# Kernel tuning notes

Measured on AMD Instinct MI355X. Metric: run time of the kernel, lower is better.

Reference implementation:

```python
import jax, jax.numpy as jnp
import numpy as np

D2 = 200  # 2*100 hardcoded in BiAttentionLayer.__init__
NEG = -10000000.0


def masked_softmax(v, m):
    # Faithful to the torch masked_softmax: softmax(v * m), re-mask, renormalize.
    r = jax.nn.softmax(v * m, axis=-1)
    r = r * m
    return r / (jnp.sum(r, axis=-1, keepdims=True) + 1e-13)


def setup_inputs() -> dict:
    key = jax.random.key(0)
    k0, k1, k2, k3, k4, k5 = jax.random.split(key, 6)
    N, T, J = 64, 1024, 64
    H = jax.random.normal(k0, (N, T, D2), jnp.float32)
    U = jax.random.normal(k1, (N, J, D2), jnp.float32)
    c_mask = jax.random.randint(k2, (N, T), 0, 2).astype(jnp.float32)
    q_mask = jax.random.randint(k3, (N, J), 0, 2).astype(jnp.float32)
    w = jax.random.normal(k4, (3 * D2,), jnp.float32) * 0.05  # Linear(3*d2, 1) weight
    b = jax.random.normal(k5, (), jnp.float32) * 0.05          # Linear bias
    return {"H": H, "U": U, "c_mask": c_mask, "q_mask": q_mask, "w": w, "b": b}


def reference(H, U, c_mask, q_mask, w, b):
    # Similarity: linear over concat(h, u, h*u) decomposed so the (N,T,J,3d)
    # intermediate is never materialized (same math as the torch module).
    w_h, w_u, w_hu = w[:D2], w[D2:2 * D2], w[2 * D2:]
    S = ((H @ w_h)[:, :, None]
         + (U @ w_u)[:, None, :]
         + jnp.einsum('ntd,njd->ntj', H * w_hu, U)
         + b)  # [N,T,J]

    # C2Q: masked softmax over question dim, attend over U.
    S_t = masked_softmax(S, q_mask[:, None, :])        # [N,T,J]
    U_ = jnp.einsum('ntj,njd->ntd', S_t, U)            # [N,T,d2]

    # Q2C: replace masked values with -1e7, max over J, softmax over context dim.
    qm = q_mask[:, None, :]
    S_rep = S * qm + NEG * (1.0 - qm)                  # [N,T,J]
    S_max = jnp.max(S_rep, axis=-1)                    # [N,T]
    a = masked_softmax(S_max, c_mask)                  # [N,T]
    H_ = jnp.einsum('nt,ntd->nd', a, H)[:, None, :]    # [N,1,d2] (broadcasts over T)

    G = jnp.concatenate([H, U_, H * U_, H * H_], axis=-1)  # [N,T,4*d2]
    return G
```

## Files before the change

### kernel.cpp

```cpp
#include <hip/hip_runtime.h>
#include <stdint.h>

#define NEGV -10000000.0f

typedef __attribute__((ext_vector_type(8))) short short8;
typedef __attribute__((ext_vector_type(4))) float f32x4;

__device__ __forceinline__ ushort f2b(float f) {
    uint32_t x = __float_as_uint(f);
    uint32_t r = x + 0x7FFFu + ((x >> 16) & 1u);
    return (ushort)(r >> 16);
}
__device__ __forceinline__ float b2f(ushort u) {
    union { float f; uint32_t i; } v; v.i = ((uint32_t)u) << 16; return v.f;
}

__launch_bounds__(256)
__global__ void k0_prep(const float* __restrict__ Ug, const float* __restrict__ wg,
                        const float* __restrict__ bg,
                        ushort* __restrict__ Bf, ushort* __restrict__ Uf,
                        float* __restrict__ cW) {
    __shared__ __align__(16) float sU[64][204];
    __shared__ float sW[600];
    const int tid = threadIdx.x, lane = tid & 63, wid = tid >> 6;
    const int n = blockIdx.x;

    for (int i = tid; i < 600; i += 256) sW[i] = wg[i];
    for (int r = wid; r < 64; r += 4) {
        const float* urow = Ug + (size_t)(n * 64 + r) * 200;
        if (lane < 50) *(float4*)&sU[r][lane * 4] = *(const float4*)(urow + lane * 4);
    }
    __syncthreads();
    const float bval = bg[0];

    ushort* bfn = Bf + (size_t)n * (28 * 512);
    for (int item = tid; item < 28 * 64; item += 256) {
        int chunk = item >> 6, l2 = item & 63;
        int kc = chunk >> 2, jt = chunk & 3;
        int g2 = l2 >> 4, li2 = l2 & 15;
        int j = jt * 16 + li2;
        int d0 = kc * 32 + g2 * 8;
        short8 v;
        #pragma unroll
        for (int e = 0; e < 8; ++e) {
            int d = d0 + e;
            float bh = 0.f;
            if (d < 200) bh = sU[j][d] * sW[400 + d] + sW[d];
            v[e] = (short)f2b(bh);
        }
        *(short8*)(bfn + (size_t)item * 8) = v;
    }

    ushort* ufn = Uf + (size_t)n * (26 * 512);
    for (int item = tid; item < 26 * 64; item += 256) {
        int chunk = item >> 6, l2 = item & 63;
        int kc2 = chunk / 13, dt = chunk % 13;
        int g2 = l2 >> 4, li2 = l2 & 15;
        int d = dt * 16 + li2;
        int j0 = kc2 * 32 + g2 * 8;
        short8 v;
        #pragma unroll
        for (int e = 0; e < 8; ++e)
            v[e] = (d < 200) ? (short)f2b(sU[j0 + e][d]) : (short)0;
        *(short8*)(ufn + (size_t)item * 8) = v;
    }

    for (int r = wid; r < 64; r += 4) {
        float part = 0.f;
        for (int d = lane; d < 200; d += 64) part += sU[r][d] * sW[200 + d];
        #pragma unroll
        for (int off = 32; off >= 1; off >>= 1) part += __shfl_xor(part, off);
        if (lane == 0) cW[n * 64 + r] = part + bval;
    }
}

__launch_bounds__(64, 4)
__global__ void k13_fused(const float* __restrict__ Hg,
                          const ushort* __restrict__ Bf,
                          const float* __restrict__ cW,
                          const float* __restrict__ qmg,
                          const ushort* __restrict__ Uf,
                          float* __restrict__ SmaxWs,
                          float* __restrict__ Gout) {
    __shared__ __align__(16) ushort sHb[16][232];
    __shared__ __align__(16) ushort sP[16][80];
    __shared__ __align__(16) ushort sU2[16][208];
    const int lane = threadIdx.x;
    const int g = lane >> 4, li = lane & 15;
    const int n = blockIdx.y, t0 = blockIdx.x * 16;

    const float* Hbase = Hg + (size_t)(n * 1024 + t0) * 200;
    #pragma unroll
    for (int it = 0; it < 13; ++it) {
        int idx = lane + it * 64;
        if (idx < 800) {
            int row = idx / 50, c4 = (idx - row * 50) * 4;
            float4 h = *(const float4*)(Hbase + (size_t)row * 200 + c4);
            uint2 wv;
            wv.x = ((uint)f2b(h.y) << 16) | (uint)f2b(h.x);
            wv.y = ((uint)f2b(h.w) << 16) | (uint)f2b(h.z);
            *(uint2*)&sHb[row][c4] = wv;
        }
    }
    #pragma unroll
    for (int it = 0; it < 4; ++it) {
        int id2 = lane + it * 64;
        int row = id2 >> 4, c = id2 & 15;
        *(uint*)&sHb[row][200 + c * 2] = 0u;
    }

    const ushort* Bn = Bf + (size_t)n * (28 * 512);
    f32x4 acc[4];
    #pragma unroll
    for (int jt = 0; jt < 4; ++jt) acc[jt] = (f32x4){0.f, 0.f, 0.f, 0.f};
    const ushort* aRow = &sHb[li][g * 8];
    #pragma unroll
    for (int kc = 0; kc < 7; ++kc) {
        short8 av = *(const short8*)(aRow + kc * 32);
        #pragma unroll
        for (int jt = 0; jt < 4; ++jt) {
            short8 bv = *(const short8*)(Bn + (size_t)((kc * 4 + jt) * 64 + lane) * 8);
            acc[jt] = __builtin_amdgcn_mfma_f32_16x16x32_bf16(av, bv, acc[jt], 0, 0, 0);
        }
    }

    float cj[4], qm[4];
    #pragma unroll
    for (int jt = 0; jt < 4; ++jt) {
        cj[jt] = cW[n * 64 + jt * 16 + li];
        qm[jt] = qmg[n * 64 + jt * 16 + li];
    }
    #pragma unroll
    for (int reg = 0; reg < 4; ++reg) {
        float x[4], y[4];
        float xm = -1e30f, ym = -1e30f;
        #pragma unroll
        for (int jt = 0; jt < 4; ++jt) {
            float s = acc[jt][reg] + cj[jt];
            x[jt] = s * qm[jt];
            y[jt] = (qm[jt] != 0.f) ? s : NEGV;
            xm = fmaxf(xm, x[jt]); ym = fmaxf(ym, y[jt]);
        }
        #pragma unroll
        for (int off = 1; off <= 8; off <<= 1) {
            xm = fmaxf(xm, __shfl_xor(xm, off));
            ym = fmaxf(ym, __shfl_xor(ym, off));
        }
        float e[4], z = 0.f, zm = 0.f;
        #pragma unroll
        for (int jt = 0; jt < 4; ++jt) {
            e[jt] = __expf(x[jt] - xm);
            z += e[jt]; zm += e[jt] * qm[jt];
        }
        #pragma unroll
        for (int off = 1; off <= 8; off <<= 1) {
            z  += __shfl_xor(z, off);
            zm += __shfl_xor(zm, off);
        }
        float inv = 1.f / (zm + 1e-13f * z);
        int trow = g * 4 + reg;
        #pragma unroll
        for (int jt = 0; jt < 4; ++jt) sP[trow][jt * 16 + li] = f2b(e[jt] * qm[jt] * inv);
        if (li == 0) SmaxWs[n * 1024 + t0 + trow] = ym;
    }

    const ushort* Un = Uf + (size_t)n * (26 * 512);
    f32x4 acc2[13];
    #pragma unroll
    for (int dt = 0; dt < 13; ++dt) acc2[dt] = (f32x4){0.f, 0.f, 0.f, 0.f};
    #pragma unroll
    for (int kc2 = 0; kc2 < 2; ++kc2) {
        short8 a2 = *(const short8*)(&sP[li][kc2 * 32 + g * 8]);
        #pragma unroll
        for (int dt = 0; dt < 13; ++dt) {
            short8 bv = *(const short8*)(Un + (size_t)((kc2 * 13 + dt) * 64 + lane) * 8);
            acc2[dt] = __builtin_amdgcn_mfma_f32_16x16x32_bf16(a2, bv, acc2[dt], 0, 0, 0);
        }
    }

    #pragma unroll
    for (int dt = 0; dt < 13; ++dt) {
        int d = dt * 16 + li;
        if (d < 200) {
            #pragma unroll
            for (int reg = 0; reg < 4; ++reg)
                sU2[g * 4 + reg][d] = f2b(acc2[dt][reg]);
        }
    }

    for (int r = 0; r < 16; ++r) {
        if (lane < 50) {
            int d0 = lane * 4;
            float* orow = Gout + (size_t)(n * 1024 + t0 + r) * 800;
            uint2 uraw = *(const uint2*)&sU2[r][d0];
            uint2 hraw = *(const uint2*)&sHb[r][d0];
            f32x4 u, h;
            u[0] = b2f((ushort)(uraw.x & 0xffffu)); u[1] = b2f((ushort)(uraw.x >> 16));
            u[2] = b2f((ushort)(uraw.y & 0xffffu)); u[3] = b2f((ushort)(uraw.y >> 16));
            h[0] = b2f((ushort)(hraw.x & 0xffffu)); h[1] = b2f((ushort)(hraw.x >> 16));
            h[2] = b2f((ushort)(hraw.y & 0xffffu)); h[3] = b2f((ushort)(hraw.y >> 16));
            f32x4 hu = h * u;
            __builtin_nontemporal_store(u,  (f32x4*)(orow + 200 + d0));
            __builtin_nontemporal_store(hu, (f32x4*)(orow + 400 + d0));
        }
    }
}

__launch_bounds__(256)
__global__ void k2a_softmaxT(const float* __restrict__ cmg,
                             const float* __restrict__ SmaxWs,
                             float* __restrict__ aWs,
                             float* __restrict__ HbarWs) {
    __shared__ float red[8];
    const int tid = threadIdx.x, lane = tid & 63, wid = tid >> 6;
    const int n = blockIdx.x;

    float x[4], m[4];
    #pragma unroll
    for (int i = 0; i < 4; ++i) {
        int t = tid + 256 * i;
        float v = SmaxWs[n * 1024 + t];
        m[i] = cmg[(size_t)n * 1024 + t];
        x[i] = v * m[i];
    }
    float mx = fmaxf(fmaxf(x[0], x[1]), fmaxf(x[2], x[3]));
    #pragma unroll
    for (int off = 32; off >= 1; off >>= 1) mx = fmaxf(mx, __shfl_xor(mx, off));
    if (lane == 0) red[wid] = mx;
    __syncthreads();
    float M = fmaxf(fmaxf(red[0], red[1]), fmaxf(red[2], red[3]));
    __syncthreads();
    float e[4], z = 0.f, zm = 0.f;
    #pragma unroll
    for (int i = 0; i < 4; ++i) {
        e[i] = __expf(x[i] - M);
        z += e[i]; zm += e[i] * m[i];
    }
    #pragma unroll
    for (int off = 32; off >= 1; off >>= 1) {
        z  += __shfl_xor(z, off);
        zm += __shfl_xor(zm, off);
    }
    if (lane == 0) { red[wid] = z; red[4 + wid] = zm; }
    __syncthreads();
    float Z  = red[0] + red[1] + red[2] + red[3];
    float Zm = red[4] + red[5] + red[6] + red[7];
    float inv = 1.f / (Zm + 1e-13f * Z);
    #pragma unroll
    for (int i = 0; i < 4; ++i) aWs[n * 1024 + tid + 256 * i] = e[i] * m[i] * inv;
    if (tid < 200) HbarWs[n * 200 + tid] = 0.f;
}

__launch_bounds__(256)
__global__ void k2b_hbar(const float* __restrict__ Hg,
                         const float* __restrict__ aWs,
                         float* __restrict__ HbarWs) {
    __shared__ float sA[64];
    const int tid = threadIdx.x;
    const int n = blockIdx.y, t0 = blockIdx.x * 64;
    if (tid < 64) sA[tid] = aWs[n * 1024 + t0 + tid];
    __syncthreads();
    if (tid < 200) {
        const float* hp = Hg + (size_t)(n * 1024 + t0) * 200 + tid;
        float acc = 0.f;
        #pragma unroll 8
        for (int t = 0; t < 64; ++t) acc += sA[t] * hp[(size_t)t * 200];
        atomicAdd(HbarWs + n * 200 + tid, acc);
    }
}

__launch_bounds__(256)
__global__ void k4_hh(const float* __restrict__ Hg,
                      const float* __restrict__ HbarWs,
                      float* __restrict__ Gout) {
    __shared__ __align__(16) float sHb[200];
    const int tid = threadIdx.x, lane = tid & 63, wid = tid >> 6;
    const int n = blockIdx.y, t0 = blockIdx.x * 64;
    if (tid < 200) sHb[tid] = HbarWs[n * 200 + tid];
    __syncthreads();
    for (int r = wid; r < 64; r += 4) {
        if (lane < 50) {
            int d0 = lane * 4;
            const float* hrow = Hg + (size_t)(n * 1024 + t0 + r) * 200;
            float* orow = Gout + (size_t)(n * 1024 + t0 + r) * 800;
            f32x4 h  = *(const f32x4*)(hrow + d0);
            f32x4 hb = *(const f32x4*)&sHb[d0];
            f32x4 hh = h * hb;
            __builtin_nontemporal_store(h,  (f32x4*)(orow + d0));
            __builtin_nontemporal_store(hh, (f32x4*)(orow + 600 + d0));
        }
    }
}

extern "C" void kernel_launch(void* const* d_in, const int* in_sizes, int n_in,
                              void* d_out, int out_size, void* d_ws, size_t ws_size,
                              hipStream_t stream) {
    (void)in_sizes; (void)n_in; (void)out_size; (void)ws_size;
    const float* Hg  = (const float*)d_in[0];
    const float* Ug  = (const float*)d_in[1];
    const float* cmg = (const float*)d_in[2];
    const float* qmg = (const float*)d_in[3];
    const float* wg  = (const float*)d_in[4];
    const float* bg  = (const float*)d_in[5];
    float* Gout = (float*)d_out;

    char* ws = (char*)d_ws;
    float*  SmaxWs = (float*) (ws);
    float*  aWs    = (float*) (ws + 262144);
    float*  HbarWs = (float*) (ws + 524288);
    float*  cWs    = (float*) (ws + 575488);
    ushort* BfWs   = (ushort*)(ws + 591872);
    ushort* UfWs   = (ushort*)(ws + 2426880);

    dim3 blk256(256, 1, 1);
    k0_prep<<<dim3(64, 1, 1), blk256, 0, stream>>>(Ug, wg, bg, BfWs, UfWs, cWs);
    k13_fused<<<dim3(64, 64, 1), dim3(64, 1, 1), 0, stream>>>(Hg, BfWs, cWs, qmg,
                                                              UfWs, SmaxWs, Gout);
    k2a_softmaxT<<<dim3(64, 1, 1), blk256, 0, stream>>>(cmg, SmaxWs, aWs, HbarWs);
    k2b_hbar<<<dim3(16, 64, 1), blk256, 0, stream>>>(Hg, aWs, HbarWs);
    k4_hh<<<dim3(16, 64, 1), blk256, 0, stream>>>(Hg, HbarWs, Gout);
}
```

Baseline: 324.5 us.

## Split GEMM2 out of first kernel and fuse it with final output writer

The fused kernel now only computes the similarity GEMM and softmax probabilities. It writes the bf16 P tiles to workspace instead of also running the second GEMM and writing U_ and H*U_. A new 256-thread kernel reads P, does the P@U GEMM and writes all four output slices (H, U_, H*U_, H*H_) in one pass, replacing the old k4 kernel. The aim is full-row output writes and a lighter first kernel, at the cost of a P round-trip through memory. The B operand loads in GEMM1 are also double-buffered in registers.

```diff
diff --git a/kernel.cpp b/kernel.cpp
--- a/kernel.cpp
+++ b/kernel.cpp
@@ -75,16 +75,14 @@
 }
 
 __launch_bounds__(64, 4)
-__global__ void k13_fused(const float* __restrict__ Hg,
-                          const ushort* __restrict__ Bf,
-                          const float* __restrict__ cW,
-                          const float* __restrict__ qmg,
-                          const ushort* __restrict__ Uf,
-                          float* __restrict__ SmaxWs,
-                          float* __restrict__ Gout) {
+__global__ void kA_gemm1(const float* __restrict__ Hg,
+                         const ushort* __restrict__ Bf,
+                         const float* __restrict__ cW,
+                         const float* __restrict__ qmg,
+                         ushort* __restrict__ PfW,
+                         float* __restrict__ SmaxWs) {
     __shared__ __align__(16) ushort sHb[16][232];
     __shared__ __align__(16) ushort sP[16][80];
-    __shared__ __align__(16) ushort sU2[16][208];
     const int lane = threadIdx.x;
     const int g = lane >> 4, li = lane & 15;
     const int n = blockIdx.y, t0 = blockIdx.x * 16;
@@ -114,14 +112,24 @@
     #pragma unroll
     for (int jt = 0; jt < 4; ++jt) acc[jt] = (f32x4){0.f, 0.f, 0.f, 0.f};
     const ushort* aRow = &sHb[li][g * 8];
+
+    short8 bbuf[2][4];
+    #pragma unroll
+    for (int jt = 0; jt < 4; ++jt)
+        bbuf[0][jt] = *(const short8*)(Bn + (size_t)((0 * 4 + jt) * 64 + lane) * 8);
     #pragma unroll
     for (int kc = 0; kc < 7; ++kc) {
+        if (kc < 6) {
+            #pragma unroll
+            for (int jt = 0; jt < 4; ++jt)
+                bbuf[(kc + 1) & 1][jt] =
+                    *(const short8*)(Bn + (size_t)(((kc + 1) * 4 + jt) * 64 + lane) * 8);
+        }
         short8 av = *(const short8*)(aRow + kc * 32);
         #pragma unroll
-        for (int jt = 0; jt < 4; ++jt) {
-            short8 bv = *(const short8*)(Bn + (size_t)((kc * 4 + jt) * 64 + lane) * 8);
-            acc[jt] = __builtin_amdgcn_mfma_f32_16x16x32_bf16(av, bv, acc[jt], 0, 0, 0);
-        }
+        for (int jt = 0; jt < 4; ++jt)
+            acc[jt] = __builtin_amdgcn_mfma_f32_16x16x32_bf16(av, bbuf[kc & 1][jt],
+                                                              acc[jt], 0, 0, 0);
     }
 
     float cj[4], qm[4];
@@ -164,45 +172,11 @@
         if (li == 0) SmaxWs[n * 1024 + t0 + trow] = ym;
     }
 
-    const ushort* Un = Uf + (size_t)n * (26 * 512);
-    f32x4 acc2[13];
-    #pragma unroll
-    for (int dt = 0; dt < 13; ++dt) acc2[dt] = (f32x4){0.f, 0.f, 0.f, 0.f};
-    #pragma unroll
-    for (int kc2 = 0; kc2 < 2; ++kc2) {
-        short8 a2 = *(const short8*)(&sP[li][kc2 * 32 + g * 8]);
-        #pragma unroll
-        for (int dt = 0; dt < 13; ++dt) {
-            short8 bv = *(const short8*)(Un + (size_t)((kc2 * 13 + dt) * 64 + lane) * 8);
-            acc2[dt] = __builtin_amdgcn_mfma_f32_16x16x32_bf16(a2, bv, acc2[dt], 0, 0, 0);
-        }
-    }
-
-    #pragma unroll
-    for (int dt = 0; dt < 13; ++dt) {
-        int d = dt * 16 + li;
-        if (d < 200) {
-            #pragma unroll
-            for (int reg = 0; reg < 4; ++reg)
-                sU2[g * 4 + reg][d] = f2b(acc2[dt][reg]);
-        }
-    }
-
-    for (int r = 0; r < 16; ++r) {
-        if (lane < 50) {
-            int d0 = lane * 4;
-            float* orow = Gout + (size_t)(n * 1024 + t0 + r) * 800;
-            uint2 uraw = *(const uint2*)&sU2[r][d0];
-            uint2 hraw = *(const uint2*)&sHb[r][d0];
-            f32x4 u, h;
-            u[0] = b2f((ushort)(uraw.x & 0xffffu)); u[1] = b2f((ushort)(uraw.x >> 16));
-            u[2] = b2f((ushort)(uraw.y & 0xffffu)); u[3] = b2f((ushort)(uraw.y >> 16));
-            h[0] = b2f((ushort)(hraw.x & 0xffffu)); h[1] = b2f((ushort)(hraw.x >> 16));
-            h[2] = b2f((ushort)(hraw.y & 0xffffu)); h[3] = b2f((ushort)(hraw.y >> 16));
-            f32x4 hu = h * u;
-            __builtin_nontemporal_store(u,  (f32x4*)(orow + 200 + d0));
-            __builtin_nontemporal_store(hu, (f32x4*)(orow + 400 + d0));
-        }
+    ushort* pf = PfW + (size_t)(n * 64 + blockIdx.x) * 1024;
+    #pragma unroll
+    for (int c2 = 0; c2 < 2; ++c2) {
+        short8 v = *(const short8*)&sP[lane & 15][c2 * 32 + (lane >> 4) * 8];
+        *(short8*)(pf + c2 * 512 + lane * 8) = v;
     }
 }
 
@@ -269,24 +243,62 @@
     }
 }
 
-__launch_bounds__(256)
-__global__ void k4_hh(const float* __restrict__ Hg,
-                      const float* __restrict__ HbarWs,
-                      float* __restrict__ Gout) {
-    __shared__ __align__(16) float sHb[200];
-    const int tid = threadIdx.x, lane = tid & 63, wid = tid >> 6;
-    const int n = blockIdx.y, t0 = blockIdx.x * 64;
-    if (tid < 200) sHb[tid] = HbarWs[n * 200 + tid];
-    __syncthreads();
-    for (int r = wid; r < 64; r += 4) {
+__launch_bounds__(256, 4)
+__global__ void kB_gemm2_out(const float* __restrict__ Hg,
+                             const ushort* __restrict__ Uf,
+                             const ushort* __restrict__ PfW,
+                             const float* __restrict__ HbarWs,
+                             float* __restrict__ Gout) {
+    __shared__ __align__(16) ushort sU2[64][208];
+    const int tid = threadIdx.x, lane = tid & 63, w = tid >> 6;
+    const int g = lane >> 4, li = lane & 15;
+    const int n = blockIdx.y, r0 = blockIdx.x * 64;
+    const int tIdx = blockIdx.x * 4 + w;
+
+    const ushort* pf = PfW + (size_t)(n * 64 + tIdx) * 1024;
+    const ushort* Un = Uf + (size_t)n * (26 * 512);
+    f32x4 acc2[13];
+    #pragma unroll
+    for (int dt = 0; dt < 13; ++dt) acc2[dt] = (f32x4){0.f, 0.f, 0.f, 0.f};
+    #pragma unroll
+    for (int kc2 = 0; kc2 < 2; ++kc2) {
+        short8 a2 = *(const short8*)(pf + kc2 * 512 + lane * 8);
+        #pragma unroll
+        for (int dt = 0; dt < 13; ++dt) {
+            short8 bv = *(const short8*)(Un + (size_t)((kc2 * 13 + dt) * 64 + lane) * 8);
+            acc2[dt] = __builtin_amdgcn_mfma_f32_16x16x32_bf16(a2, bv, acc2[dt], 0, 0, 0);
+        }
+    }
+
+    #pragma unroll
+    for (int dt = 0; dt < 13; ++dt) {
+        int d = dt * 16 + li;
+        if (d < 200) {
+            #pragma unroll
+            for (int reg = 0; reg < 4; ++reg)
+                sU2[w * 16 + g * 4 + reg][d] = f2b(acc2[dt][reg]);
+        }
+    }
+
+    const int d0 = lane * 4;
+    f32x4 hbv = (f32x4){0.f, 0.f, 0.f, 0.f};
+    if (lane < 50) hbv = *(const f32x4*)(HbarWs + n * 200 + d0);
+
+    for (int rr = 0; rr < 16; ++rr) {
+        int r = w * 16 + rr;
         if (lane < 50) {
-            int d0 = lane * 4;
-            const float* hrow = Hg + (size_t)(n * 1024 + t0 + r) * 200;
-            float* orow = Gout + (size_t)(n * 1024 + t0 + r) * 800;
-            f32x4 h  = *(const f32x4*)(hrow + d0);
-            f32x4 hb = *(const f32x4*)&sHb[d0];
-            f32x4 hh = h * hb;
+            const float* hrow = Hg + (size_t)(n * 1024 + r0 + r) * 200;
+            float* orow = Gout + (size_t)(n * 1024 + r0 + r) * 800;
+            f32x4 h = *(const f32x4*)(hrow + d0);
+            uint2 uraw = *(const uint2*)&sU2[r][d0];
+            f32x4 u;
+            u[0] = b2f((ushort)(uraw.x & 0xffffu)); u[1] = b2f((ushort)(uraw.x >> 16));
+            u[2] = b2f((ushort)(uraw.y & 0xffffu)); u[3] = b2f((ushort)(uraw.y >> 16));
+            f32x4 hu = h * u;
+            f32x4 hh = h * hbv;
             __builtin_nontemporal_store(h,  (f32x4*)(orow + d0));
+            __builtin_nontemporal_store(u,  (f32x4*)(orow + 200 + d0));
+            __builtin_nontemporal_store(hu, (f32x4*)(orow + 400 + d0));
             __builtin_nontemporal_store(hh, (f32x4*)(orow + 600 + d0));
         }
     }
@@ -311,12 +323,13 @@
     float*  cWs    = (float*) (ws + 575488);
     ushort* BfWs   = (ushort*)(ws + 591872);
     ushort* UfWs   = (ushort*)(ws + 2426880);
+    ushort* PfWs   = (ushort*)(ws + 4130816);
 
     dim3 blk256(256, 1, 1);
     k0_prep<<<dim3(64, 1, 1), blk256, 0, stream>>>(Ug, wg, bg, BfWs, UfWs, cWs);
-    k13_fused<<<dim3(64, 64, 1), dim3(64, 1, 1), 0, stream>>>(Hg, BfWs, cWs, qmg,
-                                                              UfWs, SmaxWs, Gout);
+    kA_gemm1<<<dim3(64, 64, 1), dim3(64, 1, 1), 0, stream>>>(Hg, BfWs, cWs, qmg,
+                                                             PfWs, SmaxWs);
     k2a_softmaxT<<<dim3(64, 1, 1), blk256, 0, stream>>>(cmg, SmaxWs, aWs, HbarWs);
     k2b_hbar<<<dim3(16, 64, 1), blk256, 0, stream>>>(Hg, aWs, HbarWs);
-    k4_hh<<<dim3(16, 64, 1), blk256, 0, stream>>>(Hg, HbarWs, Gout);
-}
+    kB_gemm2_out<<<dim3(16, 64, 1), blk256, 0, stream>>>(Hg, UfWs, PfWs, HbarWs, Gout);
+}
```

New measurement: 309.3 us. 4.7% less time.
